# Kernel optimization log

Measured on AMD Instinct MI355X. Metric: run time of the kernel, lower is better.

The kernel has to match this reference:

```python
import jax, jax.numpy as jnp
import numpy as np

B, N, M = 2, 2048, 512          # frames, support pts/frame, target pts/frame
G = 27                          # 3*3*3 local voxel grid centers
R = 2.4                         # max_neighbour_distance
QR = 2.0 * R                    # query radius = multiplier * R
C_IN, C_RED, C_AGG, C_POST = 128, 32, 32, 128
CIG = C_RED + 9                 # per-group conv in-channels (use_xyz adds 9)
EPS = 1e-8
BN_EPS = 1e-5


def setup_inputs() -> dict:
    key = jax.random.key(0)
    ks = jax.random.split(key, 9)
    return dict(
        support_xyz=jax.random.uniform(ks[0], (B * N, 3), jnp.float32) * 10.0,
        support_features=jax.random.normal(ks[1], (B * N, C_IN), jnp.float32),
        new_xyz=jax.random.uniform(ks[2], (B * M, 3), jnp.float32) * 10.0,
        w_group=jax.random.normal(ks[3], (G, C_AGG, CIG), jnp.float32) * 0.05,
        bn1_gamma=jnp.ones((G * C_AGG,), jnp.float32),
        bn1_beta=jnp.zeros((G * C_AGG,), jnp.float32),
        bn1_mean=jax.random.normal(ks[4], (G * C_AGG,), jnp.float32) * 0.1,
        bn1_var=jax.random.uniform(ks[5], (G * C_AGG,), jnp.float32, minval=0.5, maxval=1.5),
        w_post=jax.random.normal(ks[6], (C_POST, G * C_AGG), jnp.float32) * 0.05,
        bn2_gamma=jnp.ones((C_POST,), jnp.float32),
        bn2_beta=jnp.zeros((C_POST,), jnp.float32),
        bn2_mean=jax.random.normal(ks[7], (C_POST,), jnp.float32) * 0.1,
        bn2_var=jax.random.uniform(ks[8], (C_POST,), jnp.float32, minval=0.5, maxval=1.5),
    )


def _grid_offsets():
    # voxel centers of a 3x3x3 grid spanning [-R, R] per axis: [-1.6, 0, 1.6]
    g = (jnp.arange(3, dtype=jnp.float32) + 0.5) * (2.0 * R / 3.0) - R
    gx, gy, gz = jnp.meshgrid(g, g, g, indexing='ij')
    return jnp.stack([gx.ravel(), gy.ravel(), gz.ravel()], axis=-1)  # (G,3)


def _interp_one(pts, feats, centers):
    # pts (N,3), feats (N,C_RED), centers (M,G,3) -> (M, G*CIG)
    gc = centers.reshape(M * G, 3)
    diff = gc[:, None, :] - pts[None, :, :]               # (MG,N,3)
    d2 = jnp.sum(diff * diff, axis=-1)                    # squared distances
    cheby = jnp.max(jnp.abs(diff), axis=-1)               # cube-query metric
    d2 = jnp.where(cheby <= QR, d2, jnp.inf)
    neg, idx = jax.lax.top_k(-d2, 3)                      # 3 nearest in radius
    dist = jax.lax.stop_gradient(-neg)                    # torch computes under no_grad
    idx = jax.lax.stop_gradient(idx)
    empty = ~jnp.isfinite(dist[:, :1])                    # no neighbor found
    recip = jnp.where(jnp.isfinite(dist), 1.0 / (dist + EPS), 0.0)
    w = recip / jnp.maximum(jnp.sum(recip, axis=-1, keepdims=True), EPS)
    f = jnp.einsum('mk,mkc->mc', w, feats[idx])           # weighted 3-NN interp
    local = (gc[:, None, :] - pts[idx]).reshape(M * G, 9) # local xyz offsets
    out = jnp.concatenate([f, local], axis=-1)            # (MG, CIG)
    return jnp.where(empty, 0.0, out).reshape(M, G * CIG)


def _bn(x, gamma, beta, mean, var):
    return gamma * (x - mean) * jax.lax.rsqrt(var + BN_EPS) + beta


def reference(support_xyz, support_features, new_xyz, w_group, bn1_gamma, bn1_beta,
              bn1_mean, bn1_var, w_post, bn2_gamma, bn2_beta, bn2_mean, bn2_var):
    # channel reduction: view(N, C_IN//C_RED, C_RED).sum(1)
    feats = support_features.reshape(B * N, C_IN // C_RED, C_RED).sum(axis=1)
    centers = new_xyz[:, None, :] + _grid_offsets()[None, :, :]   # (BM,G,3)
    vec = jax.vmap(_interp_one)(
        support_xyz.reshape(B, N, 3),
        feats.reshape(B, N, C_RED),
        centers.reshape(B, M, G, 3),
    ).reshape(B * M, G, CIG)
    # grouped conv1x1 (groups=G): per-voxel small GEMM
    x = jnp.einsum('mgi,goi->mgo', vec, w_group).reshape(B * M, G * C_AGG)
    x = jnp.maximum(_bn(x, bn1_gamma, bn1_beta, bn1_mean, bn1_var), 0.0)
    y = x @ w_post.T                                              # post MLP conv1x1
    return jnp.maximum(_bn(y, bn2_gamma, bn2_beta, bn2_mean, bn2_var), 0.0)
```

## Files before the change

### kernel.cpp

```cpp
#include <hip/hip_runtime.h>

#define BATCH   2
#define NPTS    2048
#define MPTS    512
#define BM_TOT  1024
#define GVOX    27
#define CRED    32
#define CIG     41
#define CAGG    32
#define GCH     864
#define CPOST   128

__global__ __launch_bounds__(256) void vpa_main(
    const float* __restrict__ sxyz,
    const float* __restrict__ sfeat,
    const float* __restrict__ nxyz,
    const float* __restrict__ wgrp,
    const float* __restrict__ g1, const float* __restrict__ b1,
    const float* __restrict__ m1, const float* __restrict__ v1,
    float* __restrict__ xout)
{
    __shared__ float spts[NPTS * 3];
    __shared__ float lvec[4][CIG];

    const int m    = blockIdx.x;
    const int b    = m >> 9;
    const int tid  = threadIdx.x;
    const int lane = tid & 63;
    const int wv   = tid >> 6;

    const float* sx = sxyz + b * (NPTS * 3);
    for (int j = tid; j < NPTS * 3; j += 256) spts[j] = sx[j];

    const float nx = nxyz[m * 3 + 0];
    const float ny = nxyz[m * 3 + 1];
    const float nz = nxyz[m * 3 + 2];
    __syncthreads();

    const float mult = 1.6000000238418579f;
    const float INF  = __builtin_inff();

    for (int t = 0; t < 7; ++t) {
        const int  g      = wv + 4 * t;
        const bool active = (g < GVOX);

        float cx = 0.f, cy = 0.f, cz = 0.f;
        float d0 = INF, d1 = INF, d2 = INF;
        int   i0 = 0x7fffffff, i1 = 0x7fffffff, i2 = 0x7fffffff;

        if (active) {
            const int gi = g / 9, rem = g - gi * 9;
            const int gj = rem / 3, gk = rem - gj * 3;
            cx = nx + (((float)gi + 0.5f) * mult - 2.4f);
            cy = ny + (((float)gj + 0.5f) * mult - 2.4f);
            cz = nz + (((float)gk + 0.5f) * mult - 2.4f);

            #pragma unroll 8
            for (int k = 0; k < 32; ++k) {
                const int p  = (k << 6) + lane;
                const int p3 = p * 3;
                const float dx = cx - spts[p3 + 0];
                const float dy = cy - spts[p3 + 1];
                const float dz = cz - spts[p3 + 2];
                float dd = __fadd_rn(__fadd_rn(__fmul_rn(dx, dx),
                                               __fmul_rn(dy, dy)),
                                     __fmul_rn(dz, dz));
                const float ch = fmaxf(fmaxf(fabsf(dx), fabsf(dy)), fabsf(dz));
                dd = (ch <= 4.8f) ? dd : INF;
                const bool c0 = dd < d0, c1 = dd < d1, c2 = dd < d2;
                d2 = c1 ? d1 : (c2 ? dd : d2);  i2 = c1 ? i1 : (c2 ? p : i2);
                d1 = c0 ? d0 : (c1 ? dd : d1);  i1 = c0 ? i0 : (c1 ? p : i1);
                d0 = c0 ? dd : d0;              i0 = c0 ? p  : i0;
            }

            for (int s = 1; s < 64; s <<= 1) {
                const float e0 = __shfl_xor(d0, s);
                const float e1 = __shfl_xor(d1, s);
                const float e2 = __shfl_xor(d2, s);
                const int   j0 = __shfl_xor(i0, s);
                const int   j1 = __shfl_xor(i1, s);
                const int   j2 = __shfl_xor(i2, s);
                {
                    const bool c0 = (e0 < d0) || (e0 == d0 && j0 < i0);
                    const bool c1 = (e0 < d1) || (e0 == d1 && j0 < i1);
                    const bool c2 = (e0 < d2) || (e0 == d2 && j0 < i2);
                    d2 = c1 ? d1 : (c2 ? e0 : d2);  i2 = c1 ? i1 : (c2 ? j0 : i2);
                    d1 = c0 ? d0 : (c1 ? e0 : d1);  i1 = c0 ? i0 : (c1 ? j0 : i1);
                    d0 = c0 ? e0 : d0;              i0 = c0 ? j0 : i0;
                }
                {
                    const bool c0 = (e1 < d0) || (e1 == d0 && j1 < i0);
                    const bool c1 = (e1 < d1) || (e1 == d1 && j1 < i1);
                    const bool c2 = (e1 < d2) || (e1 == d2 && j1 < i2);
                    d2 = c1 ? d1 : (c2 ? e1 : d2);  i2 = c1 ? i1 : (c2 ? j1 : i2);
                    d1 = c0 ? d0 : (c1 ? e1 : d1);  i1 = c0 ? i0 : (c1 ? j1 : i1);
                    d0 = c0 ? e1 : d0;              i0 = c0 ? j1 : i0;
                }
                {
                    const bool c0 = (e2 < d0) || (e2 == d0 && j2 < i0);
                    const bool c1 = (e2 < d1) || (e2 == d1 && j2 < i1);
                    const bool c2 = (e2 < d2) || (e2 == d2 && j2 < i2);
                    d2 = c1 ? d1 : (c2 ? e2 : d2);  i2 = c1 ? i1 : (c2 ? j2 : i2);
                    d1 = c0 ? d0 : (c1 ? e2 : d1);  i1 = c0 ? i0 : (c1 ? j2 : i1);
                    d0 = c0 ? e2 : d0;              i0 = c0 ? j2 : i0;
                }
            }

            const float r0 = 1.0f / (d0 + 1e-8f);
            const float r1 = 1.0f / (d1 + 1e-8f);
            const float r2 = 1.0f / (d2 + 1e-8f);
            const float rs = fmaxf((r0 + r1) + r2, 1e-8f);
            const float w0 = r0 / rs, w1 = r1 / rs, w2 = r2 / rs;
            const bool  empty = !(d0 < INF);

            const int s0 = (i0 < NPTS) ? i0 : 0;
            const int s1 = (i1 < NPTS) ? i1 : 0;
            const int s2 = (i2 < NPTS) ? i2 : 0;

            float val = 0.0f;
            if (lane < CRED) {
                const float* F  = sfeat + b * (NPTS * 128) + lane;
                const float* p0 = F + s0 * 128;
                const float* p1 = F + s1 * 128;
                const float* p2 = F + s2 * 128;
                const float f0 = ((p0[0] + p0[32]) + p0[64]) + p0[96];
                const float f1 = ((p1[0] + p1[32]) + p1[64]) + p1[96];
                const float f2 = ((p2[0] + p2[32]) + p2[64]) + p2[96];
                val = (w0 * f0 + w1 * f1) + w2 * f2;
            } else if (lane < CIG) {
                const int j  = lane - 32;
                const int k  = j / 3, ax = j - 3 * k;
                const int ik = (k == 0) ? s0 : ((k == 1) ? s1 : s2);
                const float cc = (ax == 0) ? cx : ((ax == 1) ? cy : cz);
                val = cc - spts[ik * 3 + ax];
            }
            if (empty) val = 0.0f;
            if (lane < CIG) lvec[wv][lane] = val;
        }
        __syncthreads();

        if (active && lane < CAGG) {
            const int ch = g * CAGG + lane;
            const float* wg = wgrp + ch * CIG;
            float acc = 0.f;
            #pragma unroll
            for (int i = 0; i < CIG; ++i) acc += lvec[wv][i] * wg[i];
            const float sc = g1[ch] * rsqrtf(v1[ch] + 1e-5f);
            const float xv = fmaxf(sc * (acc - m1[ch]) + b1[ch], 0.0f);
            xout[m * GCH + ch] = xv;
        }
        __syncthreads();
    }
}

__global__ __launch_bounds__(256) void vpa_post(
    const float* __restrict__ xin,
    const float* __restrict__ wp,
    const float* __restrict__ g2, const float* __restrict__ b2,
    const float* __restrict__ m2, const float* __restrict__ v2,
    float* __restrict__ out)
{
    __shared__ float xs[4 * GCH];
    __shared__ float pb[2][128][4];

    const int mb  = blockIdx.x * 4;
    const int tid = threadIdx.x;

    for (int j = tid; j < 4 * GCH; j += 256) xs[j] = xin[mb * GCH + j];
    __syncthreads();

    const int o = tid & 127;
    const int h = tid >> 7;
    const int ibase = h * (GCH / 2);
    const float* wr = wp + o * GCH + ibase;

    float a0 = 0.f, a1 = 0.f, a2 = 0.f, a3 = 0.f;
    for (int i = 0; i < GCH / 2; ++i) {
        const float w = wr[i];
        const int  ii = ibase + i;
        a0 += xs[0 * GCH + ii] * w;
        a1 += xs[1 * GCH + ii] * w;
        a2 += xs[2 * GCH + ii] * w;
        a3 += xs[3 * GCH + ii] * w;
    }
    pb[h][o][0] = a0; pb[h][o][1] = a1; pb[h][o][2] = a2; pb[h][o][3] = a3;
    __syncthreads();

    if (h == 0) {
        const float sc = g2[o] * rsqrtf(v2[o] + 1e-5f);
        const float mu = m2[o], bt = b2[o];
        #pragma unroll
        for (int mm = 0; mm < 4; ++mm) {
            const float y = pb[0][o][mm] + pb[1][o][mm];
            out[(mb + mm) * CPOST + o] = fmaxf(sc * (y - mu) + bt, 0.0f);
        }
    }
}

extern "C" void kernel_launch(void* const* d_in, const int* in_sizes, int n_in,
                              void* d_out, int out_size, void* d_ws, size_t ws_size,
                              hipStream_t stream) {
    const float* sxyz  = (const float*)d_in[0];
    const float* sfeat = (const float*)d_in[1];
    const float* nxyz  = (const float*)d_in[2];
    const float* wgrp  = (const float*)d_in[3];
    const float* g1    = (const float*)d_in[4];
    const float* b1    = (const float*)d_in[5];
    const float* m1    = (const float*)d_in[6];
    const float* v1    = (const float*)d_in[7];
    const float* wp    = (const float*)d_in[8];
    const float* g2    = (const float*)d_in[9];
    const float* b2    = (const float*)d_in[10];
    const float* m2    = (const float*)d_in[11];
    const float* v2    = (const float*)d_in[12];

    float* outp = (float*)d_out;
    float* xbuf = (float*)d_ws;

    hipLaunchKernelGGL(vpa_main, dim3(BM_TOT), dim3(256), 0, stream,
                       sxyz, sfeat, nxyz, wgrp, g1, b1, m1, v1, xbuf);
    hipLaunchKernelGGL(vpa_post, dim3(BM_TOT / 4), dim3(256), 0, stream,
                       xbuf, wp, g2, b2, m2, v2, outp);
}
```

Measured before the change: 171.5 us.

## Fold BN into weights, batch voxel scans per point load, shuffle-based group GEMM

Adds a prep kernel that folds both batch norms into transposed and scaled weights and biases in workspace. The main kernel now loads each support point from LDS once and tests it against all 7 voxels a wave owns, so the distance loop reuses loads and gains more independent work. The per-group conv uses wave shuffles instead of LDS plus block barriers. The post GEMM switches to float4 loads with a 16-lane shuffle reduction. In exchange, register pressure rises from holding 7 top-3 states, and the extra launch adds overhead.

```diff
diff --git a/kernel.cpp b/kernel.cpp
--- a/kernel.cpp
+++ b/kernel.cpp
@@ -10,18 +10,70 @@
 #define CAGG    32
 #define GCH     864
 #define CPOST   128
-
-__global__ __launch_bounds__(256) void vpa_main(
+#define QRF     4.8f
+#define MULT    1.6000000238418579f
+
+#define WS_XBUF  0
+#define WS_WT    884736
+#define WS_BB1   920160
+#define WS_WP2   921024
+#define WS_BB2   1031616
+
+__global__ __launch_bounds__(256) void vpa_prep(
+    const float* __restrict__ wgrp,
+    const float* __restrict__ g1, const float* __restrict__ b1,
+    const float* __restrict__ m1, const float* __restrict__ v1,
+    const float* __restrict__ wp,
+    const float* __restrict__ g2, const float* __restrict__ b2,
+    const float* __restrict__ m2, const float* __restrict__ v2,
+    float* __restrict__ ws)
+{
+    const int idx = blockIdx.x * 256 + threadIdx.x;
+    if (idx < 35424) {
+        const int o = idx & 31;
+        const int r = idx >> 5;
+        const int g = r / 41;
+        const int ch = g * CAGG + o;
+        const float sc = g1[ch] * rsqrtf(v1[ch] + 1e-5f);
+        ws[WS_WT + idx] = wgrp[ch * CIG + (r - g * 41)] * sc;
+    }
+    int j = idx - 35424;
+    if (j >= 0 && j < GCH) {
+        const float sc = g1[j] * rsqrtf(v1[j] + 1e-5f);
+        ws[WS_BB1 + j] = b1[j] - sc * m1[j];
+    }
+    j = idx - (35424 + GCH);
+    if (j >= 0 && j < CPOST * GCH) {
+        const int o = j / GCH;
+        const float sc = g2[o] * rsqrtf(v2[o] + 1e-5f);
+        ws[WS_WP2 + j] = wp[j] * sc;
+    }
+    j = idx - (35424 + GCH + CPOST * GCH);
+    if (j >= 0 && j < CPOST) {
+        const float sc = g2[j] * rsqrtf(v2[j] + 1e-5f);
+        ws[WS_BB2 + j] = b2[j] - sc * m2[j];
+    }
+}
+
+__device__ __forceinline__ void merge3(float& d0, float& d1, float& d2,
+                                       int& i0, int& i1, int& i2,
+                                       float e, int jj) {
+    const bool c0 = (e < d0) || (e == d0 && jj < i0);
+    const bool c1 = (e < d1) || (e == d1 && jj < i1);
+    const bool c2 = (e < d2) || (e == d2 && jj < i2);
+    d2 = c1 ? d1 : (c2 ? e : d2);  i2 = c1 ? i1 : (c2 ? jj : i2);
+    d1 = c0 ? d0 : (c1 ? e : d1);  i1 = c0 ? i0 : (c1 ? jj : i1);
+    d0 = c0 ? e : d0;              i0 = c0 ? jj : i0;
+}
+
+__global__ __launch_bounds__(256, 4) void vpa_main(
     const float* __restrict__ sxyz,
     const float* __restrict__ sfeat,
     const float* __restrict__ nxyz,
-    const float* __restrict__ wgrp,
-    const float* __restrict__ g1, const float* __restrict__ b1,
-    const float* __restrict__ m1, const float* __restrict__ v1,
+    const float* __restrict__ ws,
     float* __restrict__ xout)
 {
     __shared__ float spts[NPTS * 3];
-    __shared__ float lvec[4][CIG];
 
     const int m    = blockIdx.x;
     const int b    = m >> 9;
@@ -37,41 +89,62 @@
     const float nz = nxyz[m * 3 + 2];
     __syncthreads();
 
-    const float mult = 1.6000000238418579f;
-    const float INF  = __builtin_inff();
-
+    const float INF = __builtin_inff();
+    const float* wT  = ws + WS_WT;
+    const float* bb1 = ws + WS_BB1;
+
+    float cxa[7], cya[7], cza[7];
+    float bd[7][3];
+    int   bi[7][3];
+
+    #pragma unroll
     for (int t = 0; t < 7; ++t) {
-        const int  g      = wv + 4 * t;
-        const bool active = (g < GVOX);
-
-        float cx = 0.f, cy = 0.f, cz = 0.f;
-        float d0 = INF, d1 = INF, d2 = INF;
-        int   i0 = 0x7fffffff, i1 = 0x7fffffff, i2 = 0x7fffffff;
-
-        if (active) {
+        const int g = wv + 4 * t;
+        if (g < GVOX) {
             const int gi = g / 9, rem = g - gi * 9;
             const int gj = rem / 3, gk = rem - gj * 3;
-            cx = nx + (((float)gi + 0.5f) * mult - 2.4f);
-            cy = ny + (((float)gj + 0.5f) * mult - 2.4f);
-            cz = nz + (((float)gk + 0.5f) * mult - 2.4f);
-
-            #pragma unroll 8
-            for (int k = 0; k < 32; ++k) {
-                const int p  = (k << 6) + lane;
-                const int p3 = p * 3;
-                const float dx = cx - spts[p3 + 0];
-                const float dy = cy - spts[p3 + 1];
-                const float dz = cz - spts[p3 + 2];
-                float dd = __fadd_rn(__fadd_rn(__fmul_rn(dx, dx),
-                                               __fmul_rn(dy, dy)),
-                                     __fmul_rn(dz, dz));
-                const float ch = fmaxf(fmaxf(fabsf(dx), fabsf(dy)), fabsf(dz));
-                dd = (ch <= 4.8f) ? dd : INF;
-                const bool c0 = dd < d0, c1 = dd < d1, c2 = dd < d2;
-                d2 = c1 ? d1 : (c2 ? dd : d2);  i2 = c1 ? i1 : (c2 ? p : i2);
-                d1 = c0 ? d0 : (c1 ? dd : d1);  i1 = c0 ? i0 : (c1 ? p : i1);
-                d0 = c0 ? dd : d0;              i0 = c0 ? p  : i0;
-            }
+            cxa[t] = nx + (((float)gi + 0.5f) * MULT - 2.4f);
+            cya[t] = ny + (((float)gj + 0.5f) * MULT - 2.4f);
+            cza[t] = nz + (((float)gk + 0.5f) * MULT - 2.4f);
+        } else {
+            cxa[t] = cya[t] = cza[t] = 1e18f;
+        }
+        bd[t][0] = bd[t][1] = bd[t][2] = INF;
+        bi[t][0] = bi[t][1] = bi[t][2] = 0x7fffffff;
+    }
+
+    for (int k = 0; k < 32; ++k) {
+        const int p  = (k << 6) + lane;
+        const int p3 = p * 3;
+        const float px = spts[p3 + 0];
+        const float py = spts[p3 + 1];
+        const float pz = spts[p3 + 2];
+        #pragma unroll
+        for (int t = 0; t < 7; ++t) {
+            const float dx = cxa[t] - px;
+            const float dy = cya[t] - py;
+            const float dz = cza[t] - pz;
+            float dd = __fadd_rn(__fadd_rn(__fmul_rn(dx, dx),
+                                           __fmul_rn(dy, dy)),
+                                 __fmul_rn(dz, dz));
+            const float ch = fmaxf(fmaxf(fabsf(dx), fabsf(dy)), fabsf(dz));
+            dd = (ch <= QRF) ? dd : INF;
+            const bool c0 = dd < bd[t][0], c1 = dd < bd[t][1], c2 = dd < bd[t][2];
+            bd[t][2] = c1 ? bd[t][1] : (c2 ? dd : bd[t][2]);
+            bi[t][2] = c1 ? bi[t][1] : (c2 ? p  : bi[t][2]);
+            bd[t][1] = c0 ? bd[t][0] : (c1 ? dd : bd[t][1]);
+            bi[t][1] = c0 ? bi[t][0] : (c1 ? p  : bi[t][1]);
+            bd[t][0] = c0 ? dd : bd[t][0];
+            bi[t][0] = c0 ? p  : bi[t][0];
+        }
+    }
+
+    #pragma unroll
+    for (int t = 0; t < 7; ++t) {
+        const int g = wv + 4 * t;
+        if (g < GVOX) {
+            float d0 = bd[t][0], d1 = bd[t][1], d2 = bd[t][2];
+            int   i0 = bi[t][0], i1 = bi[t][1], i2 = bi[t][2];
 
             for (int s = 1; s < 64; s <<= 1) {
                 const float e0 = __shfl_xor(d0, s);
@@ -80,30 +153,9 @@
                 const int   j0 = __shfl_xor(i0, s);
                 const int   j1 = __shfl_xor(i1, s);
                 const int   j2 = __shfl_xor(i2, s);
-                {
-                    const bool c0 = (e0 < d0) || (e0 == d0 && j0 < i0);
-                    const bool c1 = (e0 < d1) || (e0 == d1 && j0 < i1);
-                    const bool c2 = (e0 < d2) || (e0 == d2 && j0 < i2);
-                    d2 = c1 ? d1 : (c2 ? e0 : d2);  i2 = c1 ? i1 : (c2 ? j0 : i2);
-                    d1 = c0 ? d0 : (c1 ? e0 : d1);  i1 = c0 ? i0 : (c1 ? j0 : i1);
-                    d0 = c0 ? e0 : d0;              i0 = c0 ? j0 : i0;
-                }
-                {
-                    const bool c0 = (e1 < d0) || (e1 == d0 && j1 < i0);
-                    const bool c1 = (e1 < d1) || (e1 == d1 && j1 < i1);
-                    const bool c2 = (e1 < d2) || (e1 == d2 && j1 < i2);
-                    d2 = c1 ? d1 : (c2 ? e1 : d2);  i2 = c1 ? i1 : (c2 ? j1 : i2);
-                    d1 = c0 ? d0 : (c1 ? e1 : d1);  i1 = c0 ? i0 : (c1 ? j1 : i1);
-                    d0 = c0 ? e1 : d0;              i0 = c0 ? j1 : i0;
-                }
-                {
-                    const bool c0 = (e2 < d0) || (e2 == d0 && j2 < i0);
-                    const bool c1 = (e2 < d1) || (e2 == d1 && j2 < i1);
-                    const bool c2 = (e2 < d2) || (e2 == d2 && j2 < i2);
-                    d2 = c1 ? d1 : (c2 ? e2 : d2);  i2 = c1 ? i1 : (c2 ? j2 : i2);
-                    d1 = c0 ? d0 : (c1 ? e2 : d1);  i1 = c0 ? i0 : (c1 ? j2 : i1);
-                    d0 = c0 ? e2 : d0;              i0 = c0 ? j2 : i0;
-                }
+                merge3(d0, d1, d2, i0, i1, i2, e0, j0);
+                merge3(d0, d1, d2, i0, i1, i2, e1, j1);
+                merge3(d0, d1, d2, i0, i1, i2, e2, j2);
             }
 
             const float r0 = 1.0f / (d0 + 1e-8f);
@@ -112,87 +164,104 @@
             const float rs = fmaxf((r0 + r1) + r2, 1e-8f);
             const float w0 = r0 / rs, w1 = r1 / rs, w2 = r2 / rs;
             const bool  empty = !(d0 < INF);
-
             const int s0 = (i0 < NPTS) ? i0 : 0;
             const int s1 = (i1 < NPTS) ? i1 : 0;
             const int s2 = (i2 < NPTS) ? i2 : 0;
 
-            float val = 0.0f;
+            float fval = 0.0f;
             if (lane < CRED) {
-                const float* F  = sfeat + b * (NPTS * 128) + lane;
-                const float* p0 = F + s0 * 128;
-                const float* p1 = F + s1 * 128;
-                const float* p2 = F + s2 * 128;
+                const float* Fb = sfeat + b * (NPTS * 128) + lane;
+                const float* p0 = Fb + s0 * 128;
+                const float* p1 = Fb + s1 * 128;
+                const float* p2 = Fb + s2 * 128;
                 const float f0 = ((p0[0] + p0[32]) + p0[64]) + p0[96];
                 const float f1 = ((p1[0] + p1[32]) + p1[64]) + p1[96];
                 const float f2 = ((p2[0] + p2[32]) + p2[64]) + p2[96];
-                val = (w0 * f0 + w1 * f1) + w2 * f2;
+                fval = (w0 * f0 + w1 * f1) + w2 * f2;
             } else if (lane < CIG) {
                 const int j  = lane - 32;
-                const int k  = j / 3, ax = j - 3 * k;
-                const int ik = (k == 0) ? s0 : ((k == 1) ? s1 : s2);
-                const float cc = (ax == 0) ? cx : ((ax == 1) ? cy : cz);
-                val = cc - spts[ik * 3 + ax];
-            }
-            if (empty) val = 0.0f;
-            if (lane < CIG) lvec[wv][lane] = val;
-        }
-        __syncthreads();
-
-        if (active && lane < CAGG) {
-            const int ch = g * CAGG + lane;
-            const float* wg = wgrp + ch * CIG;
-            float acc = 0.f;
-            #pragma unroll
-            for (int i = 0; i < CIG; ++i) acc += lvec[wv][i] * wg[i];
-            const float sc = g1[ch] * rsqrtf(v1[ch] + 1e-5f);
-            const float xv = fmaxf(sc * (acc - m1[ch]) + b1[ch], 0.0f);
-            xout[m * GCH + ch] = xv;
-        }
-        __syncthreads();
+                const int kk = j / 3, ax = j - 3 * kk;
+                const int ik = (kk == 0) ? s0 : ((kk == 1) ? s1 : s2);
+                const float cc = (ax == 0) ? cxa[t] : ((ax == 1) ? cya[t] : cza[t]);
+                fval = cc - spts[ik * 3 + ax];
+            }
+            if (empty) fval = 0.0f;
+
+            float acc = 0.0f;
+            const float* wrow = wT + g * (CIG * CAGG) + (lane & 31);
+            #pragma unroll
+            for (int i = 0; i < CIG; ++i) {
+                const float bc = __shfl(fval, i);
+                acc += bc * wrow[i * CAGG];
+            }
+            if (lane < CAGG) {
+                const int ch = g * CAGG + lane;
+                xout[m * GCH + ch] = fmaxf(acc + bb1[ch], 0.0f);
+            }
+        }
     }
 }
 
 __global__ __launch_bounds__(256) void vpa_post(
     const float* __restrict__ xin,
-    const float* __restrict__ wp,
-    const float* __restrict__ g2, const float* __restrict__ b2,
-    const float* __restrict__ m2, const float* __restrict__ v2,
+    const float* __restrict__ ws,
     float* __restrict__ out)
 {
-    __shared__ float xs[4 * GCH];
-    __shared__ float pb[2][128][4];
+    __shared__ __align__(16) float xs[4 * GCH];
 
     const int mb  = blockIdx.x * 4;
     const int tid = threadIdx.x;
+    const float* wp2 = ws + WS_WP2;
+    const float* bb2 = ws + WS_BB2;
 
     for (int j = tid; j < 4 * GCH; j += 256) xs[j] = xin[mb * GCH + j];
     __syncthreads();
 
-    const int o = tid & 127;
-    const int h = tid >> 7;
-    const int ibase = h * (GCH / 2);
-    const float* wr = wp + o * GCH + ibase;
-
-    float a0 = 0.f, a1 = 0.f, a2 = 0.f, a3 = 0.f;
-    for (int i = 0; i < GCH / 2; ++i) {
-        const float w = wr[i];
-        const int  ii = ibase + i;
-        a0 += xs[0 * GCH + ii] * w;
-        a1 += xs[1 * GCH + ii] * w;
-        a2 += xs[2 * GCH + ii] * w;
-        a3 += xs[3 * GCH + ii] * w;
-    }
-    pb[h][o][0] = a0; pb[h][o][1] = a1; pb[h][o][2] = a2; pb[h][o][3] = a3;
-    __syncthreads();
-
-    if (h == 0) {
-        const float sc = g2[o] * rsqrtf(v2[o] + 1e-5f);
-        const float mu = m2[o], bt = b2[o];
-        #pragma unroll
-        for (int mm = 0; mm < 4; ++mm) {
-            const float y = pb[0][o][mm] + pb[1][o][mm];
-            out[(mb + mm) * CPOST + o] = fmaxf(sc * (y - mu) + bt, 0.0f);
+    const int il = tid & 15;
+    const int og = tid >> 4;
+
+    float acc[8][4];
+    #pragma unroll
+    for (int oo = 0; oo < 8; ++oo)
+        #pragma unroll
+        for (int mm = 0; mm < 4; ++mm) acc[oo][mm] = 0.0f;
+
+    for (int jj = 0; jj < 14; ++jj) {
+        const int i4 = il + 16 * jj;
+        if (i4 < 216) {
+            const int i = i4 * 4;
+            const float4 x0 = *(const float4*)&xs[0 * GCH + i];
+            const float4 x1 = *(const float4*)&xs[1 * GCH + i];
+            const float4 x2 = *(const float4*)&xs[2 * GCH + i];
+            const float4 x3 = *(const float4*)&xs[3 * GCH + i];
+            #pragma unroll
+            for (int oo = 0; oo < 8; ++oo) {
+                const int o = oo * 16 + og;
+                const float4 w = *(const float4*)&wp2[o * GCH + i];
+                acc[oo][0] += x0.x * w.x + x0.y * w.y + x0.z * w.z + x0.w * w.w;
+                acc[oo][1] += x1.x * w.x + x1.y * w.y + x1.z * w.z + x1.w * w.w;
+                acc[oo][2] += x2.x * w.x + x2.y * w.y + x2.z * w.z + x2.w * w.w;
+                acc[oo][3] += x3.x * w.x + x3.y * w.y + x3.z * w.z + x3.w * w.w;
+            }
+        }
+    }
+
+    #pragma unroll
+    for (int s = 1; s < 16; s <<= 1)
+        #pragma unroll
+        for (int oo = 0; oo < 8; ++oo)
+            #pragma unroll
+            for (int mm = 0; mm < 4; ++mm)
+                acc[oo][mm] += __shfl_xor(acc[oo][mm], s);
+
+    if (il == 0) {
+        #pragma unroll
+        for (int oo = 0; oo < 8; ++oo) {
+            const int o = oo * 16 + og;
+            const float bias = bb2[o];
+            #pragma unroll
+            for (int mm = 0; mm < 4; ++mm)
+                out[(mb + mm) * CPOST + o] = fmaxf(acc[oo][mm] + bias, 0.0f);
         }
     }
 }
@@ -214,11 +283,14 @@
     const float* m2    = (const float*)d_in[11];
     const float* v2    = (const float*)d_in[12];
 
+    float* ws   = (float*)d_ws;
+    float* xbuf = ws + WS_XBUF;
     float* outp = (float*)d_out;
-    float* xbuf = (float*)d_ws;
-
+
+    hipLaunchKernelGGL(vpa_prep, dim3(575), dim3(256), 0, stream,
+                       wgrp, g1, b1, m1, v1, wp, g2, b2, m2, v2, ws);
     hipLaunchKernelGGL(vpa_main, dim3(BM_TOT), dim3(256), 0, stream,
-                       sxyz, sfeat, nxyz, wgrp, g1, b1, m1, v1, xbuf);
+                       sxyz, sfeat, nxyz, ws, xbuf);
     hipLaunchKernelGGL(vpa_post, dim3(BM_TOT / 4), dim3(256), 0, stream,
-                       xbuf, wp, g2, b2, m2, v2, outp);
-}
+                       xbuf, ws, outp);
+}
```

New measurement: 224.0 us. +30.6%, slower.
